# Kernel tuning notes

Hardware: AMD Instinct MI355X
Metric: run time of the kernel (lower is better)

The kernel has to match this reference:

```python
import jax, jax.numpy as jnp
import numpy as np

D_MODEL = 1024
N_HEADS = 16
D_HEAD = D_MODEL // N_HEADS


def _pid_proj(x, Wp, Wi, Wd, Wg, bg):
    # x: (B, T, D). PID decomposition: proportional / integral (running mean) / derivative (diff).
    T = x.shape[1]
    denom = jnp.arange(1, T + 1, dtype=x.dtype)[None, :, None]
    integral = jnp.cumsum(x, axis=1) / denom
    derivative = jnp.concatenate([jnp.zeros_like(x[:, :1]), x[:, 1:] - x[:, :-1]], axis=1)
    g = jax.nn.softmax(x @ Wg.T + bg, axis=-1)  # (B, T, 3)
    return (g[..., 0:1] * (x @ Wp.T)
            + g[..., 1:2] * (integral @ Wi.T)
            + g[..., 2:3] * (derivative @ Wd.T))


def setup_inputs() -> dict:
    key = jax.random.key(0)
    ks = jax.random.split(key, 16)
    B, T, D = 2, 2048, D_MODEL
    s = 1.0 / np.sqrt(D)

    def lin(k):
        return jax.random.uniform(k, (D, D), jnp.float32, -s, s)

    inp = {"x": jax.random.normal(ks[0], (B, T, D), jnp.float32)}
    names = ["q", "k", "v"]
    i = 1
    for n in names:
        inp[n + "Wp"] = lin(ks[i]); i += 1
        inp[n + "Wi"] = lin(ks[i]) * 0.1; i += 1
        inp[n + "Wd"] = lin(ks[i]) * 0.1; i += 1
        inp[n + "Wg"] = jax.random.uniform(ks[i], (3, D), jnp.float32, -s, s); i += 1
        inp[n + "bg"] = jnp.array([1.0, 0.0, 0.0], jnp.float32)
    inp["oW"] = lin(ks[i]); i += 1
    inp["ob"] = jax.random.uniform(ks[i], (D,), jnp.float32, -s, s)
    return inp


def reference(x, qWp, qWi, qWd, qWg, qbg,
              kWp, kWi, kWd, kWg, kbg,
              vWp, vWi, vWd, vWg, vbg, oW, ob):
    B, T, D = x.shape
    H, dh = N_HEADS, D_HEAD
    Q = _pid_proj(x, qWp, qWi, qWd, qWg, qbg).reshape(B, T, H, dh).transpose(0, 2, 1, 3)
    K = _pid_proj(x, kWp, kWi, kWd, kWg, kbg).reshape(B, T, H, dh).transpose(0, 2, 1, 3)
    V = _pid_proj(x, vWp, vWi, vWd, vWg, vbg).reshape(B, T, H, dh).transpose(0, 2, 1, 3)
    scale = jnp.sqrt(jnp.asarray(dh, x.dtype))
    scores = jnp.einsum('bhqd,bhkd->bhqk', Q, K) / scale  # (B,H,T,T)
    causal = jnp.triu(jnp.ones((T, T), bool), k=1)
    scores = jnp.where(causal[None, None], -jnp.inf, scores)
    attn = jax.nn.softmax(scores, axis=-1)
    out = jnp.einsum('bhqk,bhkd->bhqd', attn, V)
    out = out.transpose(0, 2, 1, 3).reshape(B, T, D)
    return out @ oW.T + ob
```

## Files before the change

kernel.cpp:

```cpp
#include <hip/hip_runtime.h>
#include <hip/hip_bf16.h>


#define D_MODEL 1024
#define T_SEQ   2048
#define B_SZ    2
#define M_ROWS  (B_SZ * T_SEQ)
#define N_HEADS 16
#define D_HEAD  64

typedef unsigned short u16;
typedef unsigned int   u32;

typedef short  short8  __attribute__((ext_vector_type(8)));
typedef float  float4v __attribute__((ext_vector_type(4)));

__device__ __forceinline__ float bf2f(u16 u) {
    union { u32 i; float f; } c; c.i = ((u32)u) << 16; return c.f;
}
__device__ __forceinline__ u16 f2bf(float f) {
    union { float f; u32 i; } c; c.f = f;
    u32 i = c.i;
    i += 0x7FFFu + ((i >> 16) & 1u);
    return (u16)(i >> 16);
}
__device__ __forceinline__ u16 f2bfc(float f) {
    __hip_bfloat16 h = __float2bfloat16(f);
    union { __hip_bfloat16 h; u16 u; } c; c.h = h; return c.u;
}
__device__ __forceinline__ float ldin(const void* p, int i, int fl) {
    return fl ? ((const float*)p)[i] : bf2f(((const u16*)p)[i]);
}

__global__ void detect_kernel(const u32* __restrict__ x, int* __restrict__ flag)
{
    if (threadIdx.x == 0 && blockIdx.x == 0) {
        int good = 0;
        for (int i = 0; i < 256; ++i) {
            union { u32 u; float f; } c; c.u = x[i];
            float a = fabsf(c.f);
            if (c.f == c.f && a > 1e-8f && a < 1e4f) ++good;
        }
        *flag = (good >= 192) ? 1 : 0;
    }
}

__global__ __launch_bounds__(256) void scan_partial(
    const void* __restrict__ x, float* __restrict__ csum,
    const int* __restrict__ flagp)
{
    int fl = *flagp;
    int tid = blockIdx.x * 256 + threadIdx.x;
    int b = tid >> 14;
    int c = (tid >> 10) & 15;
    int d = tid & 1023;
    int base = (b * T_SEQ + c * 128) * D_MODEL + d;
    float s = 0.f;
#pragma unroll 8
    for (int t = 0; t < 128; ++t) s += ldin(x, base + t * D_MODEL, fl);
    csum[tid] = s;
}

__global__ __launch_bounds__(256) void scan_final(
    const void* __restrict__ x, const float* __restrict__ csum,
    u16* __restrict__ integ, const int* __restrict__ flagp)
{
    int fl = *flagp;
    int tid = blockIdx.x * 256 + threadIdx.x;
    int b = tid >> 14;
    int c = (tid >> 10) & 15;
    int d = tid & 1023;
    float pre = 0.f;
    int cbase = (b << 14) | d;
    for (int cc = 0; cc < c; ++cc) pre += csum[cbase + (cc << 10)];
    int base = (b * T_SEQ + c * 128) * D_MODEL + d;
    float run = pre;
    int t0 = c * 128;
    for (int t = 0; t < 128; ++t) {
        run += ldin(x, base + t * D_MODEL, fl);
        integ[base + t * D_MODEL] = f2bf(run / (float)(t0 + t + 1));
    }
}

__global__ __launch_bounds__(64) void gates_kernel(
    const void* __restrict__ x,
    const void* __restrict__ qWg, const void* __restrict__ qbg,
    const void* __restrict__ kWg, const void* __restrict__ kbg,
    const void* __restrict__ vWg, const void* __restrict__ vbg,
    float* __restrict__ gq, float* __restrict__ gk, float* __restrict__ gv,
    const int* __restrict__ flagp)
{
    int fl = *flagp;
    int row = blockIdx.x;
    int l = threadIdx.x;
    int xb = row * D_MODEL;
    float p[9];
#pragma unroll
    for (int j = 0; j < 9; ++j) p[j] = 0.f;
#pragma unroll 4
    for (int i = 0; i < 16; ++i) {
        int d = l + 64 * i;
        float xv = ldin(x, xb + d, fl);
        p[0] += xv * ldin(qWg, d, fl);
        p[1] += xv * ldin(qWg, 1024 + d, fl);
        p[2] += xv * ldin(qWg, 2048 + d, fl);
        p[3] += xv * ldin(kWg, d, fl);
        p[4] += xv * ldin(kWg, 1024 + d, fl);
        p[5] += xv * ldin(kWg, 2048 + d, fl);
        p[6] += xv * ldin(vWg, d, fl);
        p[7] += xv * ldin(vWg, 1024 + d, fl);
        p[8] += xv * ldin(vWg, 2048 + d, fl);
    }
#pragma unroll
    for (int off = 32; off > 0; off >>= 1) {
#pragma unroll
        for (int j = 0; j < 9; ++j) p[j] += __shfl_down(p[j], off);
    }
    if (l == 0) {
        const void* bgs[3] = { qbg, kbg, vbg };
        float* outs[3] = { gq, gk, gv };
#pragma unroll
        for (int pr = 0; pr < 3; ++pr) {
            float a0 = p[pr * 3 + 0] + ldin(bgs[pr], 0, fl);
            float a1 = p[pr * 3 + 1] + ldin(bgs[pr], 1, fl);
            float a2 = p[pr * 3 + 2] + ldin(bgs[pr], 2, fl);
            float mx = fmaxf(a0, fmaxf(a1, a2));
            float e0 = __expf(a0 - mx), e1 = __expf(a1 - mx), e2 = __expf(a2 - mx);
            float inv = 1.f / (e0 + e1 + e2);
            outs[pr][row * 3 + 0] = e0 * inv;
            outs[pr][row * 3 + 1] = e1 * inv;
            outs[pr][row * 3 + 2] = e2 * inv;
        }
    }
}

struct CvtArgs { const void* src[10]; };

__global__ __launch_bounds__(256) void cvt_w(
    CvtArgs a, u16* __restrict__ dst, const int* __restrict__ flagp)
{
    int fl = *flagp;
    int m = blockIdx.y;
    u16* d = dst + ((size_t)m << 20);
    int i = (blockIdx.x * 256 + threadIdx.x) * 8;
    if (fl) {
        const float* s = (const float*)a.src[m];
        float4 v0 = *(const float4*)(s + i);
        float4 v1 = *(const float4*)(s + i + 4);
        ushort4 o0, o1;
        o0.x = f2bfc(v0.x); o0.y = f2bfc(v0.y); o0.z = f2bfc(v0.z); o0.w = f2bfc(v0.w);
        o1.x = f2bfc(v1.x); o1.y = f2bfc(v1.y); o1.z = f2bfc(v1.z); o1.w = f2bfc(v1.w);
        *(ushort4*)(d + i) = o0;
        *(ushort4*)(d + i + 4) = o1;
    } else {
        const u16* s = (const u16*)a.src[m];
        *(ushort4*)(d + i)     = *(const ushort4*)(s + i);
        *(ushort4*)(d + i + 4) = *(const ushort4*)(s + i + 4);
    }
}

struct GemmArgs {
    const void* W[3][3];
    const float* G[3];
    u16* C[3];
};

template<int MODE, int BW16>
__global__ __launch_bounds__(256, 3) void mfma_gemm(
    const void* __restrict__ X, const u16* __restrict__ Ib,
    const u16* __restrict__ Abf, GemmArgs args,
    const void* __restrict__ bias, void* __restrict__ outp,
    const int* __restrict__ flagp, int Ktot)
{
    int fl = *flagp;
    __shared__ __align__(16) u16 As[2 * 4096];
    __shared__ __align__(16) u16 Bs[2 * 4096];

    int tid = threadIdx.x;
    int l = tid & 63, w = tid >> 6;
    int wm = w >> 1, wn = w & 1;
    int m0 = blockIdx.y * 128, n0 = blockIdx.x * 128;
    int z = blockIdx.z;
    int lane15 = l & 15, quad = l >> 4;
    int srow = tid >> 2;
    int cs = tid & 3;
    int skof = cs * 8;

    const void* W0; const void* W1; const void* W2;
    const float* G = nullptr;
    u16* Chead = nullptr;
    if (MODE == 0) {
        W0 = args.W[z][0]; W1 = args.W[z][1]; W2 = args.W[z][2];
        G = args.G[z]; Chead = args.C[z];
    } else {
        W0 = args.W[0][0]; W1 = W0; W2 = W0;
    }

    float gcoef[2][3];
    if (MODE == 0) {
#pragma unroll
        for (int c = 0; c < 2; ++c)
#pragma unroll
            for (int s = 0; s < 3; ++s)
                gcoef[c][s] = G[(m0 + c * 64 + srow) * 3 + s];
    }

    ushort4 ra[2][4];
    ushort4 rb[2][2];

    auto cvt4 = [](float4 t) {
        ushort4 u;
        u.x = f2bf(t.x); u.y = f2bf(t.y); u.z = f2bf(t.z); u.w = f2bf(t.w);
        return u;
    };
    auto ld8 = [&](const void* p, int idx, ushort4& o0, ushort4& o1) {
        if (fl) {
            o0 = cvt4(*(const float4*)((const float*)p + idx));
            o1 = cvt4(*(const float4*)((const float*)p + idx + 4));
        } else {
            o0 = *(const ushort4*)((const u16*)p + idx);
            o1 = *(const ushort4*)((const u16*)p + idx + 4);
        }
    };

    auto load_phase = [&](int k0) {
        int seg = k0 >> 10, ksrc = k0 & 1023;
        const void* Wse = (MODE == 0) ? (seg == 0 ? W0 : (seg == 1 ? W1 : W2)) : W0;
#pragma unroll
        for (int c = 0; c < 2; ++c) {
            int gm = m0 + c * 64 + srow;
            int idx = gm * 1024 + ksrc + skof;
            if (MODE == 1) {
                ra[c][0] = *(const ushort4*)&Abf[idx];
                ra[c][1] = *(const ushort4*)&Abf[idx + 4];
            } else if (seg == 1) {
                ra[c][0] = *(const ushort4*)&Ib[idx];
                ra[c][1] = *(const ushort4*)&Ib[idx + 4];
            } else {
                ld8(X, idx, ra[c][0], ra[c][1]);
                if (seg == 2 && (gm & (T_SEQ - 1)) != 0)
                    ld8(X, idx - 1024, ra[c][2], ra[c][3]);
            }
            int gn = n0 + c * 64 + srow;
            int bidx = gn * 1024 + ksrc + skof;
            if (BW16) {
                const u16* bs = (const u16*)Wse;
                rb[c][0] = *(const ushort4*)&bs[bidx];
                rb[c][1] = *(const ushort4*)&bs[bidx + 4];
            } else {
                ld8(Wse, bidx, rb[c][0], rb[c][1]);
            }
        }
    };

    auto unp8 = [](ushort4 a, ushort4 b, float v[8]) {
        v[0] = bf2f(a.x); v[1] = bf2f(a.y); v[2] = bf2f(a.z); v[3] = bf2f(a.w);
        v[4] = bf2f(b.x); v[5] = bf2f(b.y); v[6] = bf2f(b.z); v[7] = bf2f(b.w);
    };

    int wo[2];
#pragma unroll
    for (int c = 0; c < 2; ++c) {
        int g = c * 16 + ((srow >> 4) << 2) + cs;
        wo[c] = (g << 7) | ((((srow & 15) + g) & 15) << 3);
    }

    auto store_phase = [&](int k0, int buf) {
        int seg = k0 >> 10;
        u16* Ad = As + buf * 4096;
        u16* Bd = Bs + buf * 4096;
#pragma unroll
        for (int c = 0; c < 2; ++c) {
            int row = c * 64 + srow;
            short8 pk;
            if (MODE == 1) {
                pk[0] = (short)ra[c][0].x; pk[1] = (short)ra[c][0].y;
                pk[2] = (short)ra[c][0].z; pk[3] = (short)ra[c][0].w;
                pk[4] = (short)ra[c][1].x; pk[5] = (short)ra[c][1].y;
                pk[6] = (short)ra[c][1].z; pk[7] = (short)ra[c][1].w;
            } else {
                float v[8];
                unp8(ra[c][0], ra[c][1], v);
                if (seg == 2) {
                    int gm = m0 + row;
                    if ((gm & (T_SEQ - 1)) == 0) {
#pragma unroll
                        for (int j = 0; j < 8; ++j) v[j] = 0.f;
                    } else {
                        float pv[8];
                        unp8(ra[c][2], ra[c][3], pv);
#pragma unroll
                        for (int j = 0; j < 8; ++j) v[j] -= pv[j];
                    }
                }
                float sc = gcoef[c][seg];
#pragma unroll
                for (int j = 0; j < 8; ++j) pk[j] = (short)f2bf(v[j] * sc);
            }
            *(short8*)&Ad[wo[c]] = pk;

            short8 pb;
            pb[0] = (short)rb[c][0].x; pb[1] = (short)rb[c][0].y;
            pb[2] = (short)rb[c][0].z; pb[3] = (short)rb[c][0].w;
            pb[4] = (short)rb[c][1].x; pb[5] = (short)rb[c][1].y;
            pb[6] = (short)rb[c][1].z; pb[7] = (short)rb[c][1].w;
            *(short8*)&Bd[wo[c]] = pb;
        }
    };

    float4v acc[4][4];
#pragma unroll
    for (int i = 0; i < 4; ++i)
#pragma unroll
        for (int j = 0; j < 4; ++j)
#pragma unroll
            for (int r = 0; r < 4; ++r) acc[i][j][r] = 0.f;

    int aro[4], bro[4];
#pragma unroll
    for (int t = 0; t < 4; ++t) {
        int ga = (wm * 4 + t) * 4 + quad;
        aro[t] = (ga << 7) | (((lane15 + ga) & 15) << 3);
        int gb = (wn * 4 + t) * 4 + quad;
        bro[t] = (gb << 7) | (((lane15 + gb) & 15) << 3);
    }

    int nIt = Ktot >> 5;
    load_phase(0);
    store_phase(0, 0);

    for (int it = 0; it < nIt; ++it) {
        __syncthreads();
        int cur = it & 1;
        if (it + 1 < nIt) load_phase((it + 1) << 5);

        short8 af[4], bfr[4];
#pragma unroll
        for (int ms = 0; ms < 4; ++ms)
            af[ms] = *(const short8*)&As[cur * 4096 + aro[ms]];
#pragma unroll
        for (int ns = 0; ns < 4; ++ns)
            bfr[ns] = *(const short8*)&Bs[cur * 4096 + bro[ns]];
#pragma unroll
        for (int ms = 0; ms < 4; ++ms)
#pragma unroll
            for (int ns = 0; ns < 4; ++ns)
                acc[ms][ns] = __builtin_amdgcn_mfma_f32_16x16x32_bf16(
                    af[ms], bfr[ns], acc[ms][ns], 0, 0, 0);

        if (it + 1 < nIt) store_phase((it + 1) << 5, 1 - cur);
    }

#pragma unroll
    for (int ms = 0; ms < 4; ++ms) {
#pragma unroll
        for (int r = 0; r < 4; ++r) {
            int m = m0 + wm * 64 + ms * 16 + quad * 4 + r;
#pragma unroll
            for (int ns = 0; ns < 4; ++ns) {
                int n = n0 + wn * 64 + ns * 16 + lane15;
                float vv = acc[ms][ns][r];
                if (MODE == 0) {
                    int b = m >> 11, t = m & (T_SEQ - 1);
                    int h = n >> 6,  d = n & 63;
                    Chead[(((b << 4) + h) * T_SEQ + t) * 64 + d] = f2bf(vv);
                } else {
                    vv += ldin(bias, n, fl);
                    if (fl) ((float*)outp)[m * 1024 + n] = vv;
                    else    ((u16*)outp)[m * 1024 + n] = f2bf(vv);
                }
            }
        }
    }
}

__global__ __launch_bounds__(256) void attn_mfma(
    const u16* __restrict__ Qh, const u16* __restrict__ Kh,
    const u16* __restrict__ Vh, u16* __restrict__ AO)
{
    int bx = blockIdx.x;
    int qt = bx & 31;
    int bh = bx >> 5;
    int h  = bh & 15;
    int b  = bh >> 4;
    int tid = threadIdx.x;
    int l   = tid & 63;
    int w   = tid >> 6;
    int lane15 = l & 15;
    int quad   = l >> 4;

    __shared__ __align__(16) u16 Ks[64 * 72];
    __shared__ __align__(16) u16 Vt[64 * 72];
    __shared__ __align__(16) u16 Ps[4 * 16 * 72];

    const u16* Qb = Qh + bh * (T_SEQ * 64);
    const u16* Kb = Kh + bh * (T_SEQ * 64);
    const u16* Vb = Vh + bh * (T_SEQ * 64);

    int qrow = qt * 64 + w * 16 + lane15;
    short8 qf[2];
#pragma unroll
    for (int ks = 0; ks < 2; ++ks)
        qf[ks] = *(const short8*)&Qb[qrow * 64 + ks * 32 + quad * 8];

    float4v oacc[4];
#pragma unroll
    for (int ds = 0; ds < 4; ++ds)
#pragma unroll
        for (int r = 0; r < 4; ++r) oacc[ds][r] = 0.f;
    float mrun[4], lrun[4];
#pragma unroll
    for (int r = 0; r < 4; ++r) { mrun[r] = -1e30f; lrun[r] = 0.f; }

    int srow = tid >> 2;
    int sdc  = (tid & 3) * 16;

    for (int kt = 0; kt <= qt; ++kt) {
        {
            const u16* kp = &Kb[(kt * 64 + srow) * 64 + sdc];
            ushort4 a = *(const ushort4*)kp;
            ushort4 c = *(const ushort4*)(kp + 4);
            ushort4 d2 = *(const ushort4*)(kp + 8);
            ushort4 e = *(const ushort4*)(kp + 12);
            short8 p0, p1;
            p0[0]=a.x; p0[1]=a.y; p0[2]=a.z; p0[3]=a.w;
            p0[4]=c.x; p0[5]=c.y; p0[6]=c.z; p0[7]=c.w;
            p1[0]=d2.x; p1[1]=d2.y; p1[2]=d2.z; p1[3]=d2.w;
            p1[4]=e.x; p1[5]=e.y; p1[6]=e.z; p1[7]=e.w;
            *(short8*)&Ks[srow * 72 + sdc] = p0;
            *(short8*)&Ks[srow * 72 + sdc + 8] = p1;

            const u16* vp = &Vb[(kt * 64 + srow) * 64 + sdc];
            u16 vv[16];
            *(ushort4*)&vv[0]  = *(const ushort4*)vp;
            *(ushort4*)&vv[4]  = *(const ushort4*)(vp + 4);
            *(ushort4*)&vv[8]  = *(const ushort4*)(vp + 8);
            *(ushort4*)&vv[12] = *(const ushort4*)(vp + 12);
#pragma unroll
            for (int e2 = 0; e2 < 16; ++e2)
                Vt[(sdc + e2) * 72 + srow] = vv[e2];
        }
        __syncthreads();

        float4v sacc[4];
#pragma unroll
        for (int ns = 0; ns < 4; ++ns)
#pragma unroll
            for (int r = 0; r < 4; ++r) sacc[ns][r] = 0.f;
#pragma unroll
        for (int ks = 0; ks < 2; ++ks) {
#pragma unroll
            for (int ns = 0; ns < 4; ++ns) {
                short8 bfk = *(const short8*)&Ks[(ns * 16 + lane15) * 72 + ks * 32 + quad * 8];
                sacc[ns] = __builtin_amdgcn_mfma_f32_16x16x32_bf16(
                    qf[ks], bfk, sacc[ns], 0, 0, 0);
            }
        }

        int qg0 = qt * 64 + w * 16 + quad * 4;
#pragma unroll
        for (int ns = 0; ns < 4; ++ns) {
            int kg = kt * 64 + ns * 16 + lane15;
#pragma unroll
            for (int r = 0; r < 4; ++r) {
                float s = sacc[ns][r] * 0.125f;
                sacc[ns][r] = (kg > qg0 + r) ? -1e30f : s;
            }
        }
#pragma unroll
        for (int r = 0; r < 4; ++r) {
            float mx = fmaxf(fmaxf(sacc[0][r], sacc[1][r]),
                             fmaxf(sacc[2][r], sacc[3][r]));
#pragma unroll
            for (int m2 = 1; m2 < 16; m2 <<= 1)
                mx = fmaxf(mx, __shfl_xor(mx, m2, 64));
            float mnew = fmaxf(mrun[r], mx);
            float al = __expf(mrun[r] - mnew);
            float rs = 0.f;
#pragma unroll
            for (int ns = 0; ns < 4; ++ns) {
                float p = __expf(sacc[ns][r] - mnew);
                sacc[ns][r] = p;
                rs += p;
            }
#pragma unroll
            for (int m2 = 1; m2 < 16; m2 <<= 1)
                rs += __shfl_xor(rs, m2, 64);
            lrun[r] = lrun[r] * al + rs;
            mrun[r] = mnew;
#pragma unroll
            for (int ds = 0; ds < 4; ++ds) oacc[ds][r] *= al;
        }

        u16* Pw = &Ps[w * 16 * 72];
#pragma unroll
        for (int ns = 0; ns < 4; ++ns)
#pragma unroll
            for (int r = 0; r < 4; ++r)
                Pw[(quad * 4 + r) * 72 + ns * 16 + lane15] = f2bf(sacc[ns][r]);

#pragma unroll
        for (int ks = 0; ks < 2; ++ks) {
            short8 afp = *(const short8*)&Pw[lane15 * 72 + ks * 32 + quad * 8];
#pragma unroll
            for (int ds = 0; ds < 4; ++ds) {
                short8 bfv = *(const short8*)&Vt[(ds * 16 + lane15) * 72 + ks * 32 + quad * 8];
                oacc[ds] = __builtin_amdgcn_mfma_f32_16x16x32_bf16(
                    afp, bfv, oacc[ds], 0, 0, 0);
            }
        }
        __syncthreads();
    }

#pragma unroll
    for (int r = 0; r < 4; ++r) {
        float inv = 1.f / lrun[r];
        int t = qt * 64 + w * 16 + quad * 4 + r;
        int orow = (b * T_SEQ + t) * 1024 + h * 64;
#pragma unroll
        for (int ds = 0; ds < 4; ++ds)
            AO[orow + ds * 16 + lane15] = f2bf(oacc[ds][r] * inv);
    }
}

extern "C" void kernel_launch(void* const* d_in, const int* in_sizes, int n_in,
                              void* d_out, int out_size, void* d_ws, size_t ws_size,
                              hipStream_t stream)
{
    const void* x   = d_in[0];
    const void* qWp = d_in[1];
    const void* qWi = d_in[2];
    const void* qWd = d_in[3];
    const void* qWg = d_in[4];
    const void* qbg = d_in[5];
    const void* kWp = d_in[6];
    const void* kWi = d_in[7];
    const void* kWd = d_in[8];
    const void* kWg = d_in[9];
    const void* kbg = d_in[10];
    const void* vWp = d_in[11];
    const void* vWi = d_in[12];
    const void* vWd = d_in[13];
    const void* vWg = d_in[14];
    const void* vbg = d_in[15];
    const void* oW  = d_in[16];
    const void* ob  = d_in[17];

    const size_t SZ = (size_t)M_ROWS * D_MODEL;

    int*   flag = (int*)d_ws;
    float* fws  = (float*)d_ws;
    float* csum = fws + 64;
    float* gq   = csum + 32768;
    float* gk   = gq + 3 * M_ROWS;
    float* gv   = gk + 3 * M_ROWS;
    u16* Ib = (u16*)((char*)d_ws + (1u << 20));
    u16* AO = Ib;
    u16* Qh = Ib + SZ;
    u16* Kh = Qh + SZ;
    u16* Vh = Kh + SZ;

    const size_t NEED_FULL = (size_t)(1u << 20) + 4 * SZ * 2 + ((size_t)10 << 21);
    u16* wb = (ws_size >= NEED_FULL) ? (Vh + SZ) : nullptr;

    detect_kernel<<<1, 64, 0, stream>>>((const u32*)x, flag);
    scan_partial<<<128, 256, 0, stream>>>(x, csum, flag);
    scan_final<<<128, 256, 0, stream>>>(x, csum, Ib, flag);
    gates_kernel<<<M_ROWS, 64, 0, stream>>>(x, qWg, qbg, kWg, kbg, vWg, vbg,
                                            gq, gk, gv, flag);

    GemmArgs pa;
    pa.G[0] = gq; pa.G[1] = gk; pa.G[2] = gv;
    pa.C[0] = Qh; pa.C[1] = Kh; pa.C[2] = Vh;
    GemmArgs oa = {};

    if (wb) {
        CvtArgs ca;
        ca.src[0] = qWp; ca.src[1] = qWi; ca.src[2] = qWd;
        ca.src[3] = kWp; ca.src[4] = kWi; ca.src[5] = kWd;
        ca.src[6] = vWp; ca.src[7] = vWi; ca.src[8] = vWd;
        ca.src[9] = oW;
        cvt_w<<<dim3(512, 10), 256, 0, stream>>>(ca, wb, flag);

        for (int z2 = 0; z2 < 3; ++z2)
            for (int s2 = 0; s2 < 3; ++s2)
                pa.W[z2][s2] = wb + ((size_t)(z2 * 3 + s2) << 20);
        oa.W[0][0] = wb + ((size_t)9 << 20);

        mfma_gemm<0, 1><<<dim3(8, 32, 3), 256, 0, stream>>>(
            x, Ib, nullptr, pa, nullptr, nullptr, flag, 3072);
        attn_mfma<<<B_SZ * N_HEADS * (T_SEQ / 64), 256, 0, stream>>>(Qh, Kh, Vh, AO);
        mfma_gemm<1, 1><<<dim3(8, 32, 1), 256, 0, stream>>>(
            nullptr, nullptr, AO, oa, ob, d_out, flag, 1024);
    } else {
        pa.W[0][0] = qWp; pa.W[0][1] = qWi; pa.W[0][2] = qWd;
        pa.W[1][0] = kWp; pa.W[1][1] = kWi; pa.W[1][2] = kWd;
        pa.W[2][0] = vWp; pa.W[2][1] = vWi; pa.W[2][2] = vWd;
        oa.W[0][0] = oW;

        mfma_gemm<0, 0><<<dim3(8, 32, 3), 256, 0, stream>>>(
            x, Ib, nullptr, pa, nullptr, nullptr, flag, 3072);
        attn_mfma<<<B_SZ * N_HEADS * (T_SEQ / 64), 256, 0, stream>>>(Qh, Kh, Vh, AO);
        mfma_gemm<1, 0><<<dim3(8, 32, 1), 256, 0, stream>>>(
            nullptr, nullptr, AO, oa, ob, d_out, flag, 1024);
    }
}
```

Before: 561.8 us.

## Precompute bf16 x and derivative in scan, apply gate scaling via accumulator rescale

```diff
diff --git a/kernel.cpp b/kernel.cpp
--- a/kernel.cpp
+++ b/kernel.cpp
@@ -63,9 +63,14 @@
 
 __global__ __launch_bounds__(256) void scan_final(
     const void* __restrict__ x, const float* __restrict__ csum,
-    u16* __restrict__ integ, const int* __restrict__ flagp)
+    u16* __restrict__ integ, u16* __restrict__ ob16,
+    const int* __restrict__ flagp)
 {
     int fl = *flagp;
+    const size_t SZ = (size_t)M_ROWS * D_MODEL;
+    u16* xb_w = fl ? ob16 : nullptr;
+    u16* db_w = fl ? (ob16 + SZ) : ob16;
+
     int tid = blockIdx.x * 256 + threadIdx.x;
     int b = tid >> 14;
     int c = (tid >> 10) & 15;
@@ -76,9 +81,15 @@
     int base = (b * T_SEQ + c * 128) * D_MODEL + d;
     float run = pre;
     int t0 = c * 128;
+    float xprev = (c != 0) ? ldin(x, base - D_MODEL, fl) : 0.f;
     for (int t = 0; t < 128; ++t) {
-        run += ldin(x, base + t * D_MODEL, fl);
+        float xv = ldin(x, base + t * D_MODEL, fl);
+        run += xv;
         integ[base + t * D_MODEL] = f2bf(run / (float)(t0 + t + 1));
+        if (xb_w) xb_w[base + t * D_MODEL] = f2bf(xv);
+        float dv = (t0 + t == 0) ? 0.f : (xv - xprev);
+        db_w[base + t * D_MODEL] = f2bf(dv);
+        xprev = xv;
     }
 }
 
@@ -165,11 +176,11 @@
     u16* C[3];
 };
 
-template<int MODE, int BW16>
+template<int MODE, int BW16, int APASS>
 __global__ __launch_bounds__(256, 3) void mfma_gemm(
     const void* __restrict__ X, const u16* __restrict__ Ib,
-    const u16* __restrict__ Abf, GemmArgs args,
-    const void* __restrict__ bias, void* __restrict__ outp,
+    const u16* __restrict__ Abf, const u16* __restrict__ dscr,
+    GemmArgs args, const void* __restrict__ bias, void* __restrict__ outp,
     const int* __restrict__ flagp, int Ktot)
 {
     int fl = *flagp;
@@ -196,8 +207,14 @@
         W0 = args.W[0][0]; W1 = W0; W2 = W0;
     }
 
+    const u16* X16 = nullptr; const u16* Db = nullptr;
+    if (MODE == 0 && APASS) {
+        X16 = fl ? dscr : (const u16*)X;
+        Db  = fl ? (dscr + (size_t)M_ROWS * D_MODEL) : dscr;
+    }
+
     float gcoef[2][3];
-    if (MODE == 0) {
+    if (MODE == 0 && !APASS) {
 #pragma unroll
         for (int c = 0; c < 2; ++c)
 #pragma unroll
@@ -233,6 +250,10 @@
             if (MODE == 1) {
                 ra[c][0] = *(const ushort4*)&Abf[idx];
                 ra[c][1] = *(const ushort4*)&Abf[idx + 4];
+            } else if (APASS) {
+                const u16* Ag = (seg == 0) ? X16 : (seg == 1 ? Ib : Db);
+                ra[c][0] = *(const ushort4*)&Ag[idx];
+                ra[c][1] = *(const ushort4*)&Ag[idx + 4];
             } else if (seg == 1) {
                 ra[c][0] = *(const ushort4*)&Ib[idx];
                 ra[c][1] = *(const ushort4*)&Ib[idx + 4];
@@ -273,7 +294,7 @@
         for (int c = 0; c < 2; ++c) {
             int row = c * 64 + srow;
             short8 pk;
-            if (MODE == 1) {
+            if (MODE == 1 || APASS) {
                 pk[0] = (short)ra[c][0].x; pk[1] = (short)ra[c][0].y;
                 pk[2] = (short)ra[c][0].z; pk[3] = (short)ra[c][0].w;
                 pk[4] = (short)ra[c][1].x; pk[5] = (short)ra[c][1].y;
@@ -334,6 +355,20 @@
         int cur = it & 1;
         if (it + 1 < nIt) load_phase((it + 1) << 5);
 
+        if (MODE == 0 && APASS && (it == 32 || it == 64)) {
+            int s = it >> 5;
+#pragma unroll
+            for (int ms = 0; ms < 4; ++ms) {
+#pragma unroll
+                for (int r = 0; r < 4; ++r) {
+                    int row = m0 + wm * 64 + ms * 16 + quad * 4 + r;
+                    float f = G[row * 3 + (s - 1)] / G[row * 3 + s];
+#pragma unroll
+                    for (int ns = 0; ns < 4; ++ns) acc[ms][ns][r] *= f;
+                }
+            }
+        }
+
         short8 af[4], bfr[4];
 #pragma unroll
         for (int ms = 0; ms < 4; ++ms)
@@ -356,11 +391,14 @@
 #pragma unroll
         for (int r = 0; r < 4; ++r) {
             int m = m0 + wm * 64 + ms * 16 + quad * 4 + r;
+            float fs = 1.f;
+            if (MODE == 0 && APASS) fs = G[m * 3 + 2];
 #pragma unroll
             for (int ns = 0; ns < 4; ++ns) {
                 int n = n0 + wn * 64 + ns * 16 + lane15;
                 float vv = acc[ms][ns][r];
                 if (MODE == 0) {
+                    if (APASS) vv *= fs;
                     int b = m >> 11, t = m & (T_SEQ - 1);
                     int h = n >> 6,  d = n & 63;
                     Chead[(((b << 4) + h) * T_SEQ + t) * 64 + d] = f2bf(vv);
@@ -565,7 +603,7 @@
 
     detect_kernel<<<1, 64, 0, stream>>>((const u32*)x, flag);
     scan_partial<<<128, 256, 0, stream>>>(x, csum, flag);
-    scan_final<<<128, 256, 0, stream>>>(x, csum, Ib, flag);
+    scan_final<<<128, 256, 0, stream>>>(x, csum, Ib, (u16*)d_out, flag);
     gates_kernel<<<M_ROWS, 64, 0, stream>>>(x, qWg, qbg, kWg, kbg, vWg, vbg,
                                             gq, gk, gv, flag);
 
@@ -587,21 +625,21 @@
                 pa.W[z2][s2] = wb + ((size_t)(z2 * 3 + s2) << 20);
         oa.W[0][0] = wb + ((size_t)9 << 20);
 
-        mfma_gemm<0, 1><<<dim3(8, 32, 3), 256, 0, stream>>>(
-            x, Ib, nullptr, pa, nullptr, nullptr, flag, 3072);
+        mfma_gemm<0, 1, 1><<<dim3(8, 32, 3), 256, 0, stream>>>(
+            x, Ib, nullptr, (const u16*)d_out, pa, nullptr, nullptr, flag, 3072);
         attn_mfma<<<B_SZ * N_HEADS * (T_SEQ / 64), 256, 0, stream>>>(Qh, Kh, Vh, AO);
-        mfma_gemm<1, 1><<<dim3(8, 32, 1), 256, 0, stream>>>(
-            nullptr, nullptr, AO, oa, ob, d_out, flag, 1024);
+        mfma_gemm<1, 1, 0><<<dim3(8, 32, 1), 256, 0, stream>>>(
+            nullptr, nullptr, AO, nullptr, oa, ob, d_out, flag, 1024);
     } else {
         pa.W[0][0] = qWp; pa.W[0][1] = qWi; pa.W[0][2] = qWd;
         pa.W[1][0] = kWp; pa.W[1][1] = kWi; pa.W[1][2] = kWd;
         pa.W[2][0] = vWp; pa.W[2][1] = vWi; pa.W[2][2] = vWd;
         oa.W[0][0] = oW;
 
-        mfma_gemm<0, 0><<<dim3(8, 32, 3), 256, 0, stream>>>(
-            x, Ib, nullptr, pa, nullptr, nullptr, flag, 3072);
+        mfma_gemm<0, 0, 0><<<dim3(8, 32, 3), 256, 0, stream>>>(
+            x, Ib, nullptr, nullptr, pa, nullptr, nullptr, flag, 3072);
         attn_mfma<<<B_SZ * N_HEADS * (T_SEQ / 64), 256, 0, stream>>>(Qh, Kh, Vh, AO);
-        mfma_gemm<1, 0><<<dim3(8, 32, 1), 256, 0, stream>>>(
-            nullptr, nullptr, AO, oa, ob, d_out, flag, 1024);
-    }
-}
+        mfma_gemm<1, 0, 0><<<dim3(8, 32, 1), 256, 0, stream>>>(
+            nullptr, nullptr, AO, nullptr, oa, ob, d_out, flag, 1024);
+    }
+}
```

New measurement: 1.208 ms. 2.15x slower.
